# Optimization experiments

Hardware: AMD Instinct MI355X
Metric: run time of the kernel (lower is better)

Reference implementation:

```python
import jax, jax.numpy as jnp
import numpy as np

B, C, H, W = 16, 512, 32, 32
NH = 8
HD = C // NH


def setup_inputs() -> dict:
    key = jax.random.key(0)
    k1, k2, k3 = jax.random.split(key, 3)
    x = jax.random.normal(k1, (B, C, H, W), dtype=jnp.float32)
    w_qkv = jax.random.normal(k2, (3 * C, C), dtype=jnp.float32) * (1.0 / np.sqrt(C))
    w_proj = jax.random.normal(k3, (C, C), dtype=jnp.float32) * (1.0 / np.sqrt(C))
    b_proj = jnp.zeros((C,), dtype=jnp.float32)
    return {"x": x, "w_qkv": w_qkv, "w_proj": w_proj, "b_proj": b_proj}


def reference(x, w_qkv, w_proj, b_proj):
    b, c, h, w = x.shape
    n = h * w
    # 1x1 conv qkv: (3C, C) applied per pixel
    qkv = jnp.einsum('oc,bchw->bohw', w_qkv, x)  # [B, 3C, H, W]
    qkv = qkv.reshape(b, 3, NH, HD, n)           # [B, 3, nh, hd, N]
    qkv = jnp.transpose(qkv, (1, 0, 2, 4, 3))    # [3, B, nh, N, hd]
    q, k, v = qkv[0], qkv[1], qkv[2]
    scale = HD ** -0.5
    scores = jnp.einsum('bhnd,bhmd->bhnm', q, k) * scale  # [B, nh, N, N]
    attn = jax.nn.softmax(scores, axis=-1)
    out = jnp.einsum('bhnm,bhmd->bhnd', attn, v)          # [B, nh, N, hd]
    out = jnp.transpose(out, (0, 1, 3, 2)).reshape(b, c, h, w)
    # 1x1 conv proj with bias
    out = jnp.einsum('oc,bchw->bohw', w_proj, out) + b_proj[None, :, None, None]
    return out
```

## Files before the change

kernel.cpp:

```cpp
#include <hip/hip_runtime.h>
#include <hip/hip_bf16.h>
#include <math.h>

#define BB 16
#define CC 512
#define NH 8
#define HD 64
#define NN 1024
#define THREEC 1536

#define QSCALE 0.18033688f

typedef __attribute__((ext_vector_type(8))) short bf16x8;
typedef __attribute__((ext_vector_type(4))) float f32x4;
typedef __attribute__((ext_vector_type(16))) float f32x16;

#if __has_builtin(__builtin_amdgcn_exp2f)
#define EXP2F __builtin_amdgcn_exp2f
#else
#define EXP2F exp2f
#endif

#define XT_OFF 0u
#define WQ_OFF 16777216u
#define WP_OFF 18350080u
#define QB_OFF 18874368u
#define KB_OFF 35651584u
#define VT_OFF 52428800u
#define AB_OFF 69206016u

static __device__ inline unsigned short f2bf(float f) {
  union { float f; unsigned u; } v; v.f = f;
  unsigned r = v.u + 0x7fffu + ((v.u >> 16) & 1u);
  return (unsigned short)(r >> 16);
}

static __device__ inline unsigned pk2bf(float a, float b) {
#if defined(__AMDGCN__) && __has_builtin(__builtin_amdgcn_cvt_pk_bf16_f32)
  typedef __attribute__((ext_vector_type(2))) __bf16 bfp2;
  union { bfp2 v; unsigned u; } z;
  z.v = __builtin_amdgcn_cvt_pk_bf16_f32(a, b);
  return z.u;
#else
  return (unsigned)f2bf(a) | ((unsigned)f2bf(b) << 16);
#endif
}

static __device__ inline void gld_lds16(const unsigned short* g, unsigned short* l) {
  __builtin_amdgcn_global_load_lds(
      (const __attribute__((address_space(1))) unsigned int*)g,
      (__attribute__((address_space(3))) unsigned int*)l, 16, 0, 0);
}

__global__ __launch_bounds__(256) void prep_w(const float* __restrict__ wqkv,
                                              const float* __restrict__ wproj,
                                              unsigned short* __restrict__ dq,
                                              unsigned short* __restrict__ dp) {
  const size_t i8 = ((size_t)blockIdx.x * 256 + threadIdx.x) * 8;
  const float* src;
  unsigned short* dst;
  if (i8 < 786432u) { src = wqkv + i8; dst = dq + i8; }
  else              { src = wproj + (i8 - 786432u); dst = dp + (i8 - 786432u); }
  float4 a = *(const float4*)src;
  float4 b = *(const float4*)(src + 4);
  unsigned short pk[8] = {f2bf(a.x), f2bf(a.y), f2bf(a.z), f2bf(a.w),
                          f2bf(b.x), f2bf(b.y), f2bf(b.z), f2bf(b.w)};
  *(uint4*)dst = *(const uint4*)pk;
}

__global__ __launch_bounds__(256) void prep_xT(const float* __restrict__ x,
                                               unsigned short* __restrict__ xT) {
  const int b  = blockIdx.z;
  const int c0 = blockIdx.y * 64;
  const int n0 = blockIdx.x * 64;
  __shared__ float tile[64][65];
  const int t  = threadIdx.x;
  const int cl = t >> 4, n4 = (t & 15) * 4;
#pragma unroll
  for (int r = 0; r < 4; ++r) {
    float4 v = *(const float4*)&x[((size_t)b * CC + c0 + cl + 16 * r) * NN + n0 + n4];
    *(float4*)&tile[cl + 16 * r][n4] = v;
  }
  __syncthreads();
  const int nl = t >> 4, c4 = (t & 15) * 4;
#pragma unroll
  for (int r = 0; r < 4; ++r) {
    ushort4 p;
    p.x = f2bf(tile[c4 + 0][nl + 16 * r]);
    p.y = f2bf(tile[c4 + 1][nl + 16 * r]);
    p.z = f2bf(tile[c4 + 2][nl + 16 * r]);
    p.w = f2bf(tile[c4 + 3][nl + 16 * r]);
    *(ushort4*)&xT[((size_t)b * NN + n0 + nl + 16 * r) * CC + c0 + c4] = p;
  }
}

__global__ __launch_bounds__(256) void qkv_mfma(const unsigned short* __restrict__ wq,
                                                const unsigned short* __restrict__ xT,
                                                unsigned short* __restrict__ qb,
                                                unsigned short* __restrict__ kb_,
                                                unsigned short* __restrict__ vt) {
  const int b  = blockIdx.z;
  const int o0 = blockIdx.y * 128;
  const int n0 = blockIdx.x * 128;
  const int t  = threadIdx.x;
  const int w    = t >> 6;
  const int lane = t & 63;
  const int quad = lane >> 4;
  const int l16  = lane & 15;
  const int m_off = (w >> 1) * 64;
  const int n_off = (w & 1) * 64;

  __shared__ unsigned short sm[17408];
  unsigned short* As = sm;
  unsigned short* Bs = sm + 8192;

  const int which = o0 >> 9;
  const bool vmode = (which == 2);

  const int srow = lane >> 3;
  const int ssw  = ((lane & 7) ^ srow) * 8;
  const unsigned short* gA = wq + (size_t)(o0 + 32 * w + srow) * CC + ssw;
  const unsigned short* gB = xT + ((size_t)b * NN + n0 + 32 * w + srow) * CC + ssw;

  f32x4 acc[4][4] = {};

  for (int c0 = 0; c0 < CC; c0 += 64) {
    __syncthreads();
#pragma unroll
    for (int L = 0; L < 4; ++L) {
      gld_lds16(gA + (size_t)(8 * L) * CC + c0, &As[(32 * w + 8 * L) * 64]);
      gld_lds16(gB + (size_t)(8 * L) * CC + c0, &Bs[(32 * w + 8 * L) * 64]);
    }
    __syncthreads();
    const unsigned short* Af = vmode ? Bs : As;
    const unsigned short* Bf = vmode ? As : Bs;
#pragma unroll
    for (int ks = 0; ks < 2; ++ks) {
      const int ph = ((ks * 4 + quad) ^ (l16 & 7)) * 8;
      bf16x8 af[4], bfr[4];
#pragma unroll
      for (int i = 0; i < 4; ++i) {
        af[i]  = *(const bf16x8*)&Af[(m_off + 16 * i + l16) * 64 + ph];
        bfr[i] = *(const bf16x8*)&Bf[(n_off + 16 * i + l16) * 64 + ph];
      }
#pragma unroll
      for (int i = 0; i < 4; ++i)
#pragma unroll
        for (int j = 0; j < 4; ++j)
          acc[i][j] = __builtin_amdgcn_mfma_f32_16x16x32_bf16(af[i], bfr[j], acc[i][j], 0, 0, 0);
    }
  }

  __syncthreads();
  const float sc = (which == 0) ? QSCALE : 1.0f;
#pragma unroll
  for (int i = 0; i < 4; ++i) {
#pragma unroll
    for (int j = 0; j < 4; ++j) {
      const int Drow = m_off + 16 * i + quad * 4;
      const int Dcol = n_off + 16 * j + l16;
      ushort4 p;
      p.x = f2bf(acc[i][j][0] * sc);
      p.y = f2bf(acc[i][j][1] * sc);
      p.z = f2bf(acc[i][j][2] * sc);
      p.w = f2bf(acc[i][j][3] * sc);
      *(ushort4*)&sm[Dcol * 136 + Drow] = p;
    }
  }
  __syncthreads();
  const int lrow = t >> 1;
  const int half = t & 1;
  const unsigned short* src = &sm[lrow * 136 + 64 * half];
  if (!vmode) {
    const int hh = ((o0 >> 6) & 7) + half;
    unsigned short* dst = (which == 0 ? qb : kb_) +
        ((size_t)(b * NH + hh) * NN + n0 + lrow) * HD;
#pragma unroll
    for (int i = 0; i < 8; ++i) *(uint4*)(dst + 8 * i) = *(const uint4*)(src + 8 * i);
  } else {
    const int hh = ((o0 + lrow) >> 6) & 7;
    const int d  = lrow & 63;
    unsigned short* dst = vt + ((size_t)(b * NH + hh) * HD + d) * NN + n0 + 64 * half;
#pragma unroll
    for (int i = 0; i < 8; ++i) *(uint4*)(dst + 8 * i) = *(const uint4*)(src + 8 * i);
  }
}

__global__ __launch_bounds__(256) void attn_mfma(const unsigned short* __restrict__ Qg,
                                                 const unsigned short* __restrict__ Kg,
                                                 const unsigned short* __restrict__ Vtg,
                                                 unsigned short* __restrict__ attnB) {
  const int bh = blockIdx.x;
  const int b  = bh >> 3;
  const int h  = bh & 7;
  const int n0 = blockIdx.y * 128;
  const int t  = threadIdx.x;
  const int w    = t >> 6;
  const int lane = t & 63;
  const int l31  = lane & 31;
  const int hi   = lane >> 5;

  __shared__ unsigned short sm[9216];
  unsigned short* Ks = sm;
  unsigned short* Vt = sm + 4096;

  const unsigned short* qrow = Qg + ((size_t)bh * NN + n0 + w * 32 + l31) * HD + hi * 8;
  bf16x8 qf[4];
#pragma unroll
  for (int c = 0; c < 4; ++c) qf[c] = *(const bf16x8*)(qrow + 16 * c);

  const int krow = (l31 & ~12) | ((l31 & 4) << 1) | ((l31 & 8) >> 1);
  const int ksw  = krow & 7;
  const int vsw  = l31 & 7;

  f32x16 oacc[2] = {};
  float lx = 0.f, ly = 0.f;

  const int srow = lane >> 3;
  const int sgrp = (lane & 7) ^ (srow & 7);
  const unsigned short* kstage = Kg + (size_t)bh * NN * HD +
                                 (size_t)(16 * w + srow) * HD + sgrp * 8;
  const unsigned short* vstage = Vtg + (size_t)bh * HD * NN +
                                 (size_t)(16 * w + srow) * NN + sgrp * 8;
  unsigned short* ksl0 = &Ks[(16 * w) * 64];
  unsigned short* ksl1 = &Ks[(16 * w + 8) * 64];
  unsigned short* vsl0 = &Vt[(16 * w) * 64];
  unsigned short* vsl1 = &Vt[(16 * w + 8) * 64];

#pragma unroll 1
  for (int j0 = 0; j0 < NN; j0 += 64) {
    __syncthreads();
    gld_lds16(kstage + (size_t)j0 * HD, ksl0);
    gld_lds16(kstage + (size_t)(j0 + 8) * HD, ksl1);
    gld_lds16(vstage + j0, vsl0);
    gld_lds16(vstage + (size_t)8 * NN + j0, vsl1);
    __syncthreads();

#pragma unroll
    for (int kb = 0; kb < 2; ++kb) {
      f32x16 st = {};
      const unsigned short* krp = &Ks[(32 * kb + krow) * 64];
#pragma unroll
      for (int c = 0; c < 4; ++c) {
        bf16x8 kf = *(const bf16x8*)(krp + (((2 * c + hi) ^ ksw) * 8));
        st = __builtin_amdgcn_mfma_f32_32x32x16_bf16(kf, qf[c], st, 0, 0, 0);
      }
      float e[16];
#pragma unroll
      for (int i = 0; i < 8; ++i) {
        e[2 * i]     = EXP2F(st[2 * i]);
        e[2 * i + 1] = EXP2F(st[2 * i + 1]);
        lx += e[2 * i];
        ly += e[2 * i + 1];
      }
      unsigned P[8];
#pragma unroll
      for (int i = 0; i < 8; ++i) P[i] = pk2bf(e[2 * i], e[2 * i + 1]);

#pragma unroll
      for (int g = 0; g < 2; ++g) {
        union { unsigned u[4]; bf16x8 v; } cv;
        cv.u[0] = P[4 * g + 0]; cv.u[1] = P[4 * g + 1];
        cv.u[2] = P[4 * g + 2]; cv.u[3] = P[4 * g + 3];
#pragma unroll
        for (int mt = 0; mt < 2; ++mt) {
          const int vrow = 32 * mt + l31;
          bf16x8 vf = *(const bf16x8*)&Vt[vrow * 64 + (((4 * kb + 2 * g + hi) ^ vsw) * 8)];
          oacc[mt] = __builtin_amdgcn_mfma_f32_32x32x16_bf16(vf, cv.v, oacc[mt], 0, 0, 0);
        }
      }
    }
  }

  float lsum = lx + ly;
  lsum += __shfl_xor(lsum, 32);
  const float inv = 1.0f / lsum;

  __syncthreads();
  unsigned short* Es = sm + w * 2304;
#pragma unroll
  for (int mt = 0; mt < 2; ++mt) {
#pragma unroll
    for (int rr = 0; rr < 4; ++rr) {
      const int d = 32 * mt + 8 * rr + 4 * hi;
      ushort4 p;
      p.x = f2bf(oacc[mt][4 * rr + 0] * inv);
      p.y = f2bf(oacc[mt][4 * rr + 1] * inv);
      p.z = f2bf(oacc[mt][4 * rr + 2] * inv);
      p.w = f2bf(oacc[mt][4 * rr + 3] * inv);
      *(ushort4*)&Es[l31 * 72 + d] = p;
    }
  }
  const int q    = lane >> 1;
  const int half = lane & 1;
  const unsigned short* src = &Es[q * 72 + 32 * half];
  unsigned short* gdst = attnB + ((size_t)b * NN + n0 + w * 32 + q) * CC + h * HD + 32 * half;
#pragma unroll
  for (int i = 0; i < 4; ++i) *(uint4*)(gdst + 8 * i) = *(const uint4*)(src + 8 * i);
}

__global__ __launch_bounds__(256) void proj_mfma(const unsigned short* __restrict__ wp,
                                                 const unsigned short* __restrict__ aB,
                                                 const float* __restrict__ bias,
                                                 float* __restrict__ out) {
  const int b  = blockIdx.z;
  const int o0 = blockIdx.y * 128;
  const int n0 = blockIdx.x * 128;
  const int t  = threadIdx.x;
  const int w    = t >> 6;
  const int lane = t & 63;
  const int quad = lane >> 4;
  const int l16  = lane & 15;
  const int m_off = (w >> 1) * 64;
  const int n_off = (w & 1) * 64;

  __shared__ unsigned short sm[16384];
  unsigned short* As = sm;
  unsigned short* Bs = sm + 8192;

  const int srow = lane >> 3;
  const int ssw  = ((lane & 7) ^ srow) * 8;
  const unsigned short* gA = wp + (size_t)(o0 + 32 * w + srow) * CC + ssw;
  const unsigned short* gB = aB + ((size_t)b * NN + n0 + 32 * w + srow) * CC + ssw;

  f32x4 acc[4][4] = {};

  for (int c0 = 0; c0 < CC; c0 += 64) {
    __syncthreads();
#pragma unroll
    for (int L = 0; L < 4; ++L) {
      gld_lds16(gA + (size_t)(8 * L) * CC + c0, &As[(32 * w + 8 * L) * 64]);
      gld_lds16(gB + (size_t)(8 * L) * CC + c0, &Bs[(32 * w + 8 * L) * 64]);
    }
    __syncthreads();
#pragma unroll
    for (int ks = 0; ks < 2; ++ks) {
      const int ph = ((ks * 4 + quad) ^ (l16 & 7)) * 8;
      bf16x8 af[4], bfr[4];
#pragma unroll
      for (int i = 0; i < 4; ++i) {
        af[i]  = *(const bf16x8*)&As[(m_off + 16 * i + l16) * 64 + ph];
        bfr[i] = *(const bf16x8*)&Bs[(n_off + 16 * i + l16) * 64 + ph];
      }
#pragma unroll
      for (int i = 0; i < 4; ++i)
#pragma unroll
        for (int j = 0; j < 4; ++j)
          acc[i][j] = __builtin_amdgcn_mfma_f32_16x16x32_bf16(af[i], bfr[j], acc[i][j], 0, 0, 0);
    }
  }

#pragma unroll
  for (int i = 0; i < 4; ++i) {
#pragma unroll
    for (int r = 0; r < 4; ++r) {
      const int o = o0 + m_off + 16 * i + quad * 4 + r;
      const float bv = bias[o];
      float* orow = out + ((size_t)b * CC + o) * NN + n0 + n_off;
#pragma unroll
      for (int j = 0; j < 4; ++j)
        orow[16 * j + l16] = acc[i][j][r] + bv;
    }
  }
}

extern "C" void kernel_launch(void* const* d_in, const int* in_sizes, int n_in,
                              void* d_out, int out_size, void* d_ws, size_t ws_size,
                              hipStream_t stream) {
  const float* x      = (const float*)d_in[0];
  const float* w_qkv  = (const float*)d_in[1];
  const float* w_proj = (const float*)d_in[2];
  const float* b_proj = (const float*)d_in[3];
  char* wsb  = (char*)d_ws;
  float* out = (float*)d_out;

  unsigned short* xT  = (unsigned short*)(wsb + XT_OFF);
  unsigned short* wq  = (unsigned short*)(wsb + WQ_OFF);
  unsigned short* wp  = (unsigned short*)(wsb + WP_OFF);
  unsigned short* qb  = (unsigned short*)(wsb + QB_OFF);
  unsigned short* kb_ = (unsigned short*)(wsb + KB_OFF);
  unsigned short* vt  = (unsigned short*)(wsb + VT_OFF);
  unsigned short* aB  = (unsigned short*)(wsb + AB_OFF);

  prep_w<<<512, 256, 0, stream>>>(w_qkv, w_proj, wq, wp);
  prep_xT<<<dim3(16, 8, BB), 256, 0, stream>>>(x, xT);
  qkv_mfma<<<dim3(8, 12, BB), 256, 0, stream>>>(wq, xT, qb, kb_, vt);
  attn_mfma<<<dim3(BB * NH, NN / 128), 256, 0, stream>>>(qb, kb_, vt, aB);
  proj_mfma<<<dim3(8, 4, BB), 256, 0, stream>>>(wp, aB, b_proj, out);
}
```

Before: 206.4 us.

## Give each attention wave two query tiles and halve block size to 128 threads

The attention kernel now runs 2 waves per block instead of 4, and each wave handles 64 query rows (two 32-row tiles). K and V fragments read from LDS are reused across both query tiles. The LDS tile layout changes to a padded 72-element row stride with a different XOR swizzle. One wave stages all of K and the other all of V. The aim is to halve LDS read traffic per MFMA. The cost is more accumulator registers per wave and fewer waves per block to hide load latency.

```diff
diff --git a/kernel.cpp b/kernel.cpp
--- a/kernel.cpp
+++ b/kernel.cpp
@@ -186,7 +186,7 @@
   }
 }
 
-__global__ __launch_bounds__(256) void attn_mfma(const unsigned short* __restrict__ Qg,
+__global__ __launch_bounds__(128) void attn_mfma(const unsigned short* __restrict__ Qg,
                                                  const unsigned short* __restrict__ Kg,
                                                  const unsigned short* __restrict__ Vtg,
                                                  unsigned short* __restrict__ attnB) {
@@ -202,101 +202,124 @@
 
   __shared__ unsigned short sm[9216];
   unsigned short* Ks = sm;
-  unsigned short* Vt = sm + 4096;
-
-  const unsigned short* qrow = Qg + ((size_t)bh * NN + n0 + w * 32 + l31) * HD + hi * 8;
-  bf16x8 qf[4];
-#pragma unroll
-  for (int c = 0; c < 4; ++c) qf[c] = *(const bf16x8*)(qrow + 16 * c);
+  unsigned short* Vt = sm + 4608;
+
+  const unsigned short* qbase = Qg + ((size_t)bh * NN + n0 + 64 * w) * HD + hi * 8;
+  bf16x8 qf[2][4];
+#pragma unroll
+  for (int qs = 0; qs < 2; ++qs)
+#pragma unroll
+    for (int c = 0; c < 4; ++c)
+      qf[qs][c] = *(const bf16x8*)(qbase + (size_t)(32 * qs + l31) * HD + 16 * c);
 
   const int krow = (l31 & ~12) | ((l31 & 4) << 1) | ((l31 & 8) >> 1);
-  const int ksw  = krow & 7;
-  const int vsw  = l31 & 7;
-
-  f32x16 oacc[2] = {};
-  float lx = 0.f, ly = 0.f;
-
-  const int srow = lane >> 3;
-  const int sgrp = (lane & 7) ^ (srow & 7);
-  const unsigned short* kstage = Kg + (size_t)bh * NN * HD +
-                                 (size_t)(16 * w + srow) * HD + sgrp * 8;
-  const unsigned short* vstage = Vtg + (size_t)bh * HD * NN +
-                                 (size_t)(16 * w + srow) * NN + sgrp * 8;
-  unsigned short* ksl0 = &Ks[(16 * w) * 64];
-  unsigned short* ksl1 = &Ks[(16 * w + 8) * 64];
-  unsigned short* vsl0 = &Vt[(16 * w) * 64];
-  unsigned short* vsl1 = &Vt[(16 * w + 8) * 64];
+  const int fk   = ((krow >> 3) & 1) * 4;
+  const int fv   = ((l31 >> 3) & 1) * 4;
+
+  f32x16 oacc[2][2] = {};
+  float lacc[2] = {0.f, 0.f};
+
+  int sOff[9];
+#pragma unroll
+  for (int s = 0; s < 9; ++s) {
+    const int idx = 64 * s + lane;
+    const int row = (idx * 7282) >> 16;
+    const int scol = idx - 9 * row;
+    const int fR  = ((row >> 3) & 1) * 4;
+    const int g   = (scol < 8) ? (scol ^ fR) : 0;
+    sOff[s] = (w == 0) ? (row * HD + g * 8) : (row * NN + g * 8);
+  }
+  const unsigned short* gsrc = (w == 0)
+      ? (Kg + (size_t)bh * NN * HD)
+      : (Vtg + (size_t)bh * HD * NN);
+  const int tstep = (w == 0) ? 64 * HD : 64;
+  unsigned short* sdst = (w == 0) ? Ks : Vt;
 
 #pragma unroll 1
   for (int j0 = 0; j0 < NN; j0 += 64) {
     __syncthreads();
-    gld_lds16(kstage + (size_t)j0 * HD, ksl0);
-    gld_lds16(kstage + (size_t)(j0 + 8) * HD, ksl1);
-    gld_lds16(vstage + j0, vsl0);
-    gld_lds16(vstage + (size_t)8 * NN + j0, vsl1);
+#pragma unroll
+    for (int s = 0; s < 9; ++s) gld_lds16(gsrc + sOff[s], sdst + 512 * s);
+    gsrc += tstep;
     __syncthreads();
 
 #pragma unroll
     for (int kb = 0; kb < 2; ++kb) {
-      f32x16 st = {};
-      const unsigned short* krp = &Ks[(32 * kb + krow) * 64];
-#pragma unroll
-      for (int c = 0; c < 4; ++c) {
-        bf16x8 kf = *(const bf16x8*)(krp + (((2 * c + hi) ^ ksw) * 8));
-        st = __builtin_amdgcn_mfma_f32_32x32x16_bf16(kf, qf[c], st, 0, 0, 0);
+      bf16x8 kf[4];
+      const unsigned short* krp = Ks + (32 * kb + krow) * 72;
+#pragma unroll
+      for (int c = 0; c < 4; ++c)
+        kf[c] = *(const bf16x8*)(krp + ((2 * c + hi) ^ fk) * 8);
+      bf16x8 vf[2][2];
+#pragma unroll
+      for (int mt = 0; mt < 2; ++mt) {
+        const unsigned short* vrp = Vt + (32 * mt + l31) * 72;
+#pragma unroll
+        for (int g = 0; g < 2; ++g)
+          vf[g][mt] = *(const bf16x8*)(vrp + ((4 * kb + 2 * g + hi) ^ fv) * 8);
       }
-      float e[16];
-#pragma unroll
-      for (int i = 0; i < 8; ++i) {
-        e[2 * i]     = EXP2F(st[2 * i]);
-        e[2 * i + 1] = EXP2F(st[2 * i + 1]);
-        lx += e[2 * i];
-        ly += e[2 * i + 1];
-      }
-      unsigned P[8];
-#pragma unroll
-      for (int i = 0; i < 8; ++i) P[i] = pk2bf(e[2 * i], e[2 * i + 1]);
-
-#pragma unroll
-      for (int g = 0; g < 2; ++g) {
-        union { unsigned u[4]; bf16x8 v; } cv;
-        cv.u[0] = P[4 * g + 0]; cv.u[1] = P[4 * g + 1];
-        cv.u[2] = P[4 * g + 2]; cv.u[3] = P[4 * g + 3];
-#pragma unroll
-        for (int mt = 0; mt < 2; ++mt) {
-          const int vrow = 32 * mt + l31;
-          bf16x8 vf = *(const bf16x8*)&Vt[vrow * 64 + (((4 * kb + 2 * g + hi) ^ vsw) * 8)];
-          oacc[mt] = __builtin_amdgcn_mfma_f32_32x32x16_bf16(vf, cv.v, oacc[mt], 0, 0, 0);
+#pragma unroll
+      for (int qs = 0; qs < 2; ++qs) {
+        f32x16 st = {};
+#pragma unroll
+        for (int c = 0; c < 4; ++c)
+          st = __builtin_amdgcn_mfma_f32_32x32x16_bf16(kf[c], qf[qs][c], st, 0, 0, 0);
+        float e[16];
+#pragma unroll
+        for (int r = 0; r < 16; ++r) { e[r] = EXP2F(st[r]); lacc[qs] += e[r]; }
+        unsigned P[8];
+#pragma unroll
+        for (int i = 0; i < 8; ++i) P[i] = pk2bf(e[2 * i], e[2 * i + 1]);
+#pragma unroll
+        for (int g = 0; g < 2; ++g) {
+          union { unsigned u[4]; bf16x8 v; } cv;
+          cv.u[0] = P[4 * g + 0]; cv.u[1] = P[4 * g + 1];
+          cv.u[2] = P[4 * g + 2]; cv.u[3] = P[4 * g + 3];
+#pragma unroll
+          for (int mt = 0; mt < 2; ++mt)
+            oacc[qs][mt] = __builtin_amdgcn_mfma_f32_32x32x16_bf16(
+                vf[g][mt], cv.v, oacc[qs][mt], 0, 0, 0);
         }
       }
     }
   }
 
-  float lsum = lx + ly;
-  lsum += __shfl_xor(lsum, 32);
-  const float inv = 1.0f / lsum;
+  float inv[2];
+#pragma unroll
+  for (int qs = 0; qs < 2; ++qs) {
+    float l = lacc[qs];
+    l += __shfl_xor(l, 32);
+    inv[qs] = 1.0f / l;
+  }
 
   __syncthreads();
-  unsigned short* Es = sm + w * 2304;
-#pragma unroll
-  for (int mt = 0; mt < 2; ++mt) {
-#pragma unroll
-    for (int rr = 0; rr < 4; ++rr) {
-      const int d = 32 * mt + 8 * rr + 4 * hi;
-      ushort4 p;
-      p.x = f2bf(oacc[mt][4 * rr + 0] * inv);
-      p.y = f2bf(oacc[mt][4 * rr + 1] * inv);
-      p.z = f2bf(oacc[mt][4 * rr + 2] * inv);
-      p.w = f2bf(oacc[mt][4 * rr + 3] * inv);
-      *(ushort4*)&Es[l31 * 72 + d] = p;
-    }
-  }
-  const int q    = lane >> 1;
+  unsigned short* Es = sm + w * 4608;
+#pragma unroll
+  for (int qs = 0; qs < 2; ++qs) {
+#pragma unroll
+    for (int mt = 0; mt < 2; ++mt) {
+#pragma unroll
+      for (int rr = 0; rr < 4; ++rr) {
+        const int d = 32 * mt + 8 * rr + 4 * hi;
+        ushort4 p;
+        p.x = f2bf(oacc[qs][mt][4 * rr + 0] * inv[qs]);
+        p.y = f2bf(oacc[qs][mt][4 * rr + 1] * inv[qs]);
+        p.z = f2bf(oacc[qs][mt][4 * rr + 2] * inv[qs]);
+        p.w = f2bf(oacc[qs][mt][4 * rr + 3] * inv[qs]);
+        *(ushort4*)&Es[(32 * qs + l31) * 72 + d] = p;
+      }
+    }
+  }
   const int half = lane & 1;
-  const unsigned short* src = &Es[q * 72 + 32 * half];
-  unsigned short* gdst = attnB + ((size_t)b * NN + n0 + w * 32 + q) * CC + h * HD + 32 * half;
-#pragma unroll
-  for (int i = 0; i < 4; ++i) *(uint4*)(gdst + 8 * i) = *(const uint4*)(src + 8 * i);
+#pragma unroll
+  for (int p = 0; p < 2; ++p) {
+    const int q = 32 * p + (lane >> 1);
+    const unsigned short* src = &Es[q * 72 + 32 * half];
+    unsigned short* gdst = attnB + ((size_t)b * NN + n0 + 64 * w + q) * CC +
+                           h * HD + 32 * half;
+#pragma unroll
+    for (int i = 0; i < 4; ++i) *(uint4*)(gdst + 8 * i) = *(const uint4*)(src + 8 * i);
+  }
 }
 
 __global__ __launch_bounds__(256) void proj_mfma(const unsigned short* __restrict__ wp,
@@ -385,6 +408,6 @@
   prep_w<<<512, 256, 0, stream>>>(w_qkv, w_proj, wq, wp);
   prep_xT<<<dim3(16, 8, BB), 256, 0, stream>>>(x, xT);
   qkv_mfma<<<dim3(8, 12, BB), 256, 0, stream>>>(wq, xT, qb, kb_, vt);
-  attn_mfma<<<dim3(BB * NH, NN / 128), 256, 0, stream>>>(qb, kb_, vt, aB);
+  attn_mfma<<<dim3(BB * NH, NN / 128), 128, 0, stream>>>(qb, kb_, vt, aB);
   proj_mfma<<<dim3(8, 4, BB), 256, 0, stream>>>(wp, aB, b_proj, out);
 }
```

New measurement: 213.0 us. 1.03x slower.
